# Performance work log

Hardware: AMD Instinct MI355X
Metric: run time of the kernel (lower is better)

Reference implementation:

```python
import jax, jax.numpy as jnp
import numpy as np

B = 8
C = 128          # channels
H = 1024         # sparse (hidden) channels in bottleneck
START = 128      # start_frames
SPARSE = 8192    # sparse_frames
K = 512          # k_sparse
N_UP = 6         # log2(SPARSE/START) upsample blocks
EPS = 1e-5


def conv1d(x, w, b, stride=1, pad=0):
    # x: (B, Cin, L), w: (Cout, Cin, K)
    y = jax.lax.conv_general_dilated(
        x, w, window_strides=(stride,), padding=[(pad, pad)],
        dimension_numbers=('NCW', 'OIW', 'NCW'))
    return y + b[None, :, None]


def batch_norm(x, g, beta):
    # training-mode BatchNorm1d: stats over (batch, length) per channel
    m = x.mean(axis=(0, 2), keepdims=True)
    v = x.var(axis=(0, 2), keepdims=True)
    return (x - m) * jax.lax.rsqrt(v + EPS) * g[None, :, None] + beta[None, :, None]


def lrelu(x):
    return jnp.where(x >= 0, x, 0.2 * x)


def setup_inputs() -> dict:
    key = jax.random.key(0)
    ks = jax.random.split(key, 16)
    s = 0.05
    return {
        'x': jax.random.normal(ks[0], (B, C, START), dtype=jnp.float32),
        'up_w': jax.random.normal(ks[1], (N_UP, C, C, 3), dtype=jnp.float32) * s,
        'up_b': jnp.zeros((N_UP, C), dtype=jnp.float32),
        'up_g': jnp.ones((N_UP, C), dtype=jnp.float32),
        'up_beta': jnp.zeros((N_UP, C), dtype=jnp.float32),
        'up_out_w': jax.random.normal(ks[2], (C, C, 3), dtype=jnp.float32) * s,
        'up_out_b': jnp.zeros((C,), dtype=jnp.float32),
        # SparseBottleneck 1x1 convs (stored as (out,in) matrices)
        'sb_up_w': jax.random.normal(ks[3], (H, C), dtype=jnp.float32) * s,
        'sb_up_b': jnp.zeros((H,), dtype=jnp.float32),
        'sal_w': jax.random.normal(ks[4], (H, C), dtype=jnp.float32) * s,
        'sal_b': jnp.zeros((H,), dtype=jnp.float32),
        'sb_down_w': jax.random.normal(ks[5], (C, H), dtype=jnp.float32) * s,
        'sb_down_b': jnp.zeros((C,), dtype=jnp.float32),
        'dn_w': jax.random.normal(ks[6], (3, C, C, 7), dtype=jnp.float32) * s,
        'dn_b': jnp.zeros((3, C), dtype=jnp.float32),
        'dn_g': jnp.ones((3, C), dtype=jnp.float32),
        'dn_beta': jnp.zeros((3, C), dtype=jnp.float32),
    }


def reference(x, up_w, up_b, up_g, up_beta, up_out_w, up_out_b,
              sb_up_w, sb_up_b, sal_w, sal_b, sb_down_w, sb_down_b,
              dn_w, dn_b, dn_g, dn_beta):
    # ---- ConvUpsample: 128 -> 8192 frames ----
    for i in range(N_UP):
        x = jnp.repeat(x, 2, axis=-1)
        x = conv1d(x, up_w[i], up_b[i], stride=1, pad=1)
        x = lrelu(batch_norm(x, up_g[i], up_beta[i]))
    x = conv1d(x, up_out_w, up_out_b, stride=1, pad=1)  # (B, C, 8192)

    # ---- SparseBottleneck ----
    sig = jnp.einsum('bcl,hc->bhl', x, sb_up_w) + sb_up_b[None, :, None]   # (B,H,L)
    sal = jnp.einsum('bcl,hc->bhl', x, sal_w) + sal_b[None, :, None]       # (B,H,L)
    flat = jax.nn.softmax(sal.reshape(B, -1), axis=-1)   # softmax over H*L
    vals, idx = jax.lax.top_k(flat, K)                   # (B, K)
    sparse = jnp.zeros_like(flat).at[jnp.arange(B)[:, None], idx].set(vals)
    sal = sparse.reshape(sal.shape)
    x = sig * sal                                         # gated, (B,H,L)
    x = jnp.einsum('bhl,ch->bcl', x, sb_down_w) + sb_down_b[None, :, None]

    # ---- down stack: 8192 -> 128 frames ----
    for i in range(3):
        x = conv1d(x, dn_w[i], dn_b[i], stride=4, pad=3)
        x = lrelu(x)
        x = batch_norm(x, dn_g[i], dn_beta[i])
    return x  # (B, C, 128)
```

## Files before the change

### kernel.cpp

```cpp
#include <hip/hip_runtime.h>
#include <hip/hip_bf16.h>


#define DEV_INLINE __device__ __forceinline__

constexpr int NB   = 8;
constexpr int NC   = 128;
constexpr int NH   = 1024;
constexpr int LFULL= 8192;
constexpr int KSEL = 512;
constexpr int CAP  = 32768;

typedef __attribute__((ext_vector_type(4))) float f32x4;
typedef __attribute__((ext_vector_type(8))) short bf16x8;

DEV_INLINE unsigned monoKey(float f) {
    unsigned u = __float_as_uint(f);
    return (u & 0x80000000u) ? ~u : (u | 0x80000000u);
}
DEV_INLINE float keyToF(unsigned k) {
    unsigned u = (k & 0x80000000u) ? (k ^ 0x80000000u) : ~k;
    return __uint_as_float(u);
}
DEV_INLINE unsigned monoKey16(unsigned u) {
    return (u & 0x8000u) ? ((~u) & 0xFFFFu) : (u | 0x8000u);
}
DEV_INLINE unsigned bf16r(float f) {
    unsigned u = __float_as_uint(f);
    return (u + 0x7FFFu + ((u >> 16) & 1u)) >> 16;
}
DEV_INLINE float lrelu(float v) { return v >= 0.f ? v : 0.2f * v; }
DEV_INLINE float f4c(const float4& v, int k) {
    return k == 0 ? v.x : k == 1 ? v.y : k == 2 ? v.z : v.w;
}
DEV_INLINE int swz4(int p) { return p ^ ((p >> 3) & 7); }

DEV_INLINE void loadg4(const float* __restrict__ rowp, int g0, int L, float* e) {
    if (g0 >= 0 && g0 + 4 <= L) {
        float4 v = *(const float4*)(rowp + g0);
        e[0] = v.x; e[1] = v.y; e[2] = v.z; e[3] = v.w;
    } else {
#pragma unroll
        for (int t = 0; t < 4; t++) {
            int g = g0 + t;
            e[t] = (g >= 0 && g < L) ? rowp[g] : 0.f;
        }
    }
}

__global__ __launch_bounds__(256) void prep_k(
    const float* __restrict__ up_w, const float* __restrict__ up_out_w,
    const float* __restrict__ dn_w, float* __restrict__ wprep)
{
    int idx = blockIdx.x * 256 + threadIdx.x;
    if (idx < 393216) {
        int layer = idx >> 16;
        int r0 = idx & 65535;
        int c = r0 >> 9, r = (r0 >> 7) & 3, o = r0 & 127;
        const float* wsrc = up_w + ((size_t)layer * 128 + o) * 384 + c * 3;
        float w0 = wsrc[0], w1 = wsrc[1], w2 = wsrc[2];
        wprep[idx] = (r == 0) ? w0 : (r == 1) ? (w1 + w2) : (r == 2) ? (w0 + w1) : w2;
    } else if (idx < 442368) {
        int r0 = idx - 393216;
        int c = r0 / 384, k = (r0 / 128) % 3, o = r0 & 127;
        wprep[idx] = up_out_w[((size_t)o * 128 + c) * 3 + k];
    } else {
        int r0 = idx - 442368;
        int layer = r0 / 114688;
        int r1 = r0 - layer * 114688;
        int c = r1 / 896, k = (r1 / 128) % 7, o = r1 & 127;
        wprep[idx] = dn_w[((size_t)layer * 128 + o) * 896 + c * 7 + k];
    }
}

__global__ __launch_bounds__(256) void prepA_k(
    const float* __restrict__ up_w, const float* __restrict__ up_out_w,
    unsigned short* __restrict__ afrag)
{
    int idx = blockIdx.x * 256 + threadIdx.x;
    if (idx >= 221184) return;
    int rid = idx >> 6, lane = idx & 63;
    const int r15 = lane & 15, g = lane >> 4;
    unsigned short vals[8];
    if (rid < 3072) {
        int L  = rid >> 9;
        int r0 = rid & 511;
        int f = r0 & 3, ks = (r0 >> 2) & 1, cc = (r0 >> 3) & 1;
        int wo = (r0 >> 4) & 1, half = (r0 >> 5) & 1, ptap = (r0 >> 6) & 3;
        int o = wo * 64 + f * 16 + r15;
        int cb = cc * 64 + ks * 32 + g * 8;
#pragma unroll
        for (int e = 0; e < 8; e++) {
            const float* ws = up_w + (((size_t)L * 128 + o) * 128 + (cb + e)) * 3;
            float w0 = ws[0], w1 = ws[1], w2 = ws[2];
            float v = (ptap == 0) ? w0 : (ptap == 1) ? (w1 + w2)
                    : (ptap == 2) ? (w0 + w1) : w2;
            unsigned hi = bf16r(v);
            if (half == 0) vals[e] = (unsigned short)hi;
            else vals[e] = (unsigned short)bf16r(v - __uint_as_float(hi << 16));
        }
    } else {
        int r2 = rid - 3072;
        int f = r2 & 3, ks = (r2 >> 2) & 1, cc = (r2 >> 3) & 1;
        int wo = (r2 >> 4) & 1, half = (r2 >> 5) & 1, tap = r2 >> 6;
        int o = wo * 64 + f * 16 + r15;
        int cb = cc * 64 + ks * 32 + g * 8;
#pragma unroll
        for (int e = 0; e < 8; e++) {
            float v = up_out_w[((size_t)o * 128 + (cb + e)) * 3 + tap];
            unsigned hi = bf16r(v);
            if (half == 0) vals[e] = (unsigned short)hi;
            else vals[e] = (unsigned short)bf16r(v - __uint_as_float(hi << 16));
        }
    }
    unsigned pk[4];
#pragma unroll
    for (int q = 0; q < 4; q++)
        pk[q] = (unsigned)vals[2*q] | ((unsigned)vals[2*q+1] << 16);
    *(uint4*)(afrag + (size_t)rid * 512 + lane * 8) = make_uint4(pk[0], pk[1], pk[2], pk[3]);
}

__global__ __launch_bounds__(256) void redstats_k(
    const float* __restrict__ partial, int nb, float* __restrict__ stats)
{
    const int c = threadIdx.x;
    float s0 = 0.f, s1 = 0.f, s2 = 0.f, s3 = 0.f;
    for (int i = blockIdx.x * 4; i < nb; i += gridDim.x * 4) {
        s0 += partial[(size_t)(i + 0) * 256 + c];
        s1 += partial[(size_t)(i + 1) * 256 + c];
        s2 += partial[(size_t)(i + 2) * 256 + c];
        s3 += partial[(size_t)(i + 3) * 256 + c];
    }
    float s = (s0 + s1) + (s2 + s3);
    if (s != 0.f || blockIdx.x == 0) atomicAdd(&stats[c], s);
}

template<int INMODE>
__global__ __launch_bounds__(512) void mconvU_k(
    const float* __restrict__ in, float* __restrict__ out,
    const unsigned short* __restrict__ afrag, const float* __restrict__ bias,
    const float* __restrict__ stp, const float* __restrict__ gp,
    const float* __restrict__ btp, float inv_n,
    float* __restrict__ partial, int L_in)
{
    __shared__ unsigned short Xh[66 * 64], Xl[66 * 64];
    __shared__ float scs[NC], shs[NC];
    __shared__ float sstat[256];

    const int b = blockIdx.y, tile0 = blockIdx.x * 64, tid = threadIdx.x;
    const int lane = tid & 63, wid = tid >> 6;
    const int wo = wid >> 2, par = (wid >> 1) & 1, jh = wid & 1;
    const int r15 = lane & 15, g = lane >> 4;
    const int bid = b * gridDim.x + blockIdx.x;

    if (tid < 256) sstat[tid] = 0.f;
    if (INMODE > 0) {
        for (int c = tid; c < NC; c += 512) {
            float m  = stp[c] * inv_n;
            float va = stp[NC + c] * inv_n - m * m;
            float sc = gp[c] * rsqrtf(va + 1e-5f);
            scs[c] = sc;
            shs[c] = btp[c] - m * sc;
        }
    }

    f32x4 acc[4][2];
#pragma unroll
    for (int i = 0; i < 4; i++)
#pragma unroll
        for (int j = 0; j < 2; j++) acc[i][j] = (f32x4)(0.f);

    for (int cc = 0; cc < 2; cc++) {
        __syncthreads();
        {
            int r = tid & 63;
            int l = tile0 - 1 + r;
            for (int c0 = (tid >> 6); c0 < 64; c0 += 8) {
                int c = cc * 64 + c0;
                float v = 0.f;
                if (l >= 0 && l < L_in) {
                    v = in[((size_t)b * NC + c) * L_in + l];
                    if (INMODE > 0) v = lrelu(v * scs[c] + shs[c]);
                }
                unsigned hi = bf16r(v);
                unsigned lo = bf16r(v - __uint_as_float(hi << 16));
                unsigned bo = ((unsigned)(r * 128 + c0 * 2)) ^ (((unsigned)(r & 7)) << 4);
                *(unsigned short*)((char*)Xh + bo) = (unsigned short)hi;
                *(unsigned short*)((char*)Xl + bo) = (unsigned short)lo;
            }
            if (tid < 128) {
                int r2 = 64 + (tid >> 6);
                int l2 = tile0 - 1 + r2;
                int c0 = tid & 63;
                int c = cc * 64 + c0;
                float v = 0.f;
                if (l2 >= 0 && l2 < L_in) {
                    v = in[((size_t)b * NC + c) * L_in + l2];
                    if (INMODE > 0) v = lrelu(v * scs[c] + shs[c]);
                }
                unsigned hi = bf16r(v);
                unsigned lo = bf16r(v - __uint_as_float(hi << 16));
                unsigned bo = ((unsigned)(r2 * 128 + c0 * 2)) ^ (((unsigned)(r2 & 7)) << 4);
                *(unsigned short*)((char*)Xh + bo) = (unsigned short)hi;
                *(unsigned short*)((char*)Xl + bo) = (unsigned short)lo;
            }
        }
        __syncthreads();
#pragma unroll
        for (int pt = 0; pt < 2; pt++) {
            const int ptap = par * 2 + pt;
            const int roff = (ptap == 0) ? 0 : (ptap == 3) ? 2 : 1;
#pragma unroll
            for (int combo = 0; combo < 3; combo++) {
                const int ah = (combo == 2) ? 1 : 0;
                const unsigned short* Xs = (combo == 1) ? Xl : Xh;
                bf16x8 af[8];
#pragma unroll
                for (int ks = 0; ks < 2; ks++)
#pragma unroll
                    for (int f = 0; f < 4; f++) {
                        int rec = ((((ptap * 2 + ah) * 2 + wo) * 2 + cc) * 2 + ks) * 4 + f;
                        af[ks * 4 + f] = *(const bf16x8*)(afrag + (size_t)rec * 512 + lane * 8);
                    }
#pragma unroll
                for (int ks = 0; ks < 2; ks++) {
                    bf16x8 bf_[2];
#pragma unroll
                    for (int j = 0; j < 2; j++) {
                        int row = (jh * 2 + j) * 16 + r15 + roff;
                        unsigned bo = ((unsigned)(row * 128 + ks * 64 + g * 16))
                                    ^ (((unsigned)(row & 7)) << 4);
                        bf_[j] = *(const bf16x8*)((const char*)Xs + bo);
                    }
#pragma unroll
                    for (int i = 0; i < 4; i++)
#pragma unroll
                        for (int j = 0; j < 2; j++)
                            acc[i][j] = __builtin_amdgcn_mfma_f32_16x16x32_bf16(
                                af[ks * 4 + i], bf_[j], acc[i][j], 0, 0, 0);
                }
            }
        }
    }

    const int L_out = 2 * L_in;
#pragma unroll
    for (int i = 0; i < 4; i++) {
#pragma unroll
        for (int r = 0; r < 4; r++) {
            const int o = wo * 64 + i * 16 + g * 4 + r;
            const float bv = bias[o];
            float s1 = 0.f, s2 = 0.f;
#pragma unroll
            for (int j = 0; j < 2; j++) {
                float v = acc[i][j][r] + bv;
                int lout = 2 * (tile0 + (jh * 2 + j) * 16 + r15) + par;
                out[((size_t)b * NC + o) * L_out + lout] = v;
                s1 += v; s2 += v * v;
            }
#pragma unroll
            for (int m = 1; m < 16; m <<= 1) {
                s1 += __shfl_xor(s1, m);
                s2 += __shfl_xor(s2, m);
            }
            if (r15 == 0) {
                atomicAdd(&sstat[o], s1);
                atomicAdd(&sstat[NC + o], s2);
            }
        }
    }
    __syncthreads();
    if (tid < 256) partial[(size_t)bid * 256 + tid] = sstat[tid];
}

__global__ __launch_bounds__(512) void mconvF_k(
    const float* __restrict__ in, float* __restrict__ out,
    const unsigned short* __restrict__ afrag, const float* __restrict__ bias,
    const float* __restrict__ stp, const float* __restrict__ gp,
    const float* __restrict__ btp, float inv_n,
    unsigned short* __restrict__ xtout)
{
    __shared__ unsigned short Xh[130 * 64], Xl[130 * 64];
    __shared__ float scs[NC], shs[NC];

    const int b = blockIdx.y, l0 = blockIdx.x * 128, tid = threadIdx.x;
    const int lane = tid & 63, wid = tid >> 6;
    const int wo = wid >> 2, wl = (wid & 3) * 32;
    const int r15 = lane & 15, g = lane >> 4;

    for (int c = tid; c < NC; c += 512) {
        float m  = stp[c] * inv_n;
        float va = stp[NC + c] * inv_n - m * m;
        float sc = gp[c] * rsqrtf(va + 1e-5f);
        scs[c] = sc;
        shs[c] = btp[c] - m * sc;
    }

    f32x4 acc[4][2];
#pragma unroll
    for (int i = 0; i < 4; i++)
#pragma unroll
        for (int j = 0; j < 2; j++) acc[i][j] = (f32x4)(0.f);

    for (int cc = 0; cc < 2; cc++) {
        __syncthreads();
        {
            int r = tid & 127;
            int l = l0 - 1 + r;
            for (int c0 = (tid >> 7); c0 < 64; c0 += 4) {
                int c = cc * 64 + c0;
                float v = 0.f;
                if (l >= 0 && l < LFULL) {
                    v = in[((size_t)b * NC + c) * LFULL + l];
                    v = lrelu(v * scs[c] + shs[c]);
                }
                unsigned hi = bf16r(v);
                unsigned lo = bf16r(v - __uint_as_float(hi << 16));
                unsigned bo = ((unsigned)(r * 128 + c0 * 2)) ^ (((unsigned)(r & 7)) << 4);
                *(unsigned short*)((char*)Xh + bo) = (unsigned short)hi;
                *(unsigned short*)((char*)Xl + bo) = (unsigned short)lo;
            }
            if (tid < 128) {
                int r2 = 128 + (tid >> 6);
                int l2 = l0 - 1 + r2;
                int c0 = tid & 63;
                int c = cc * 64 + c0;
                float v = 0.f;
                if (l2 >= 0 && l2 < LFULL) {
                    v = in[((size_t)b * NC + c) * LFULL + l2];
                    v = lrelu(v * scs[c] + shs[c]);
                }
                unsigned hi = bf16r(v);
                unsigned lo = bf16r(v - __uint_as_float(hi << 16));
                unsigned bo = ((unsigned)(r2 * 128 + c0 * 2)) ^ (((unsigned)(r2 & 7)) << 4);
                *(unsigned short*)((char*)Xh + bo) = (unsigned short)hi;
                *(unsigned short*)((char*)Xl + bo) = (unsigned short)lo;
            }
        }
        __syncthreads();
#pragma unroll
        for (int tap = 0; tap < 3; tap++) {
#pragma unroll
            for (int combo = 0; combo < 3; combo++) {
                const int ah = (combo == 2) ? 1 : 0;
                const unsigned short* Xs = (combo == 1) ? Xl : Xh;
                bf16x8 af[8];
#pragma unroll
                for (int ks = 0; ks < 2; ks++)
#pragma unroll
                    for (int f = 0; f < 4; f++) {
                        int rec = 3072 + ((((tap * 2 + ah) * 2 + wo) * 2 + cc) * 2 + ks) * 4 + f;
                        af[ks * 4 + f] = *(const bf16x8*)(afrag + (size_t)rec * 512 + lane * 8);
                    }
#pragma unroll
                for (int ks = 0; ks < 2; ks++) {
                    bf16x8 bf_[2];
#pragma unroll
                    for (int j = 0; j < 2; j++) {
                        int row = wl + j * 16 + r15 + tap;
                        unsigned bo = ((unsigned)(row * 128 + ks * 64 + g * 16))
                                    ^ (((unsigned)(row & 7)) << 4);
                        bf_[j] = *(const bf16x8*)((const char*)Xs + bo);
                    }
#pragma unroll
                    for (int i = 0; i < 4; i++)
#pragma unroll
                        for (int j = 0; j < 2; j++)
                            acc[i][j] = __builtin_amdgcn_mfma_f32_16x16x32_bf16(
                                af[ks * 4 + i], bf_[j], acc[i][j], 0, 0, 0);
                }
            }
        }
    }

#pragma unroll
    for (int i = 0; i < 4; i++) {
#pragma unroll
        for (int r = 0; r < 4; r++) {
            const int o = wo * 64 + i * 16 + g * 4 + r;
            const float bv = bias[o];
#pragma unroll
            for (int j = 0; j < 2; j++) {
                float v = acc[i][j][r] + bv;
                int l = l0 + wl + j * 16 + r15;
                out[((size_t)b * NC + o) * LFULL + l] = v;
                xtout[((size_t)b * LFULL + l) * NC + o] = (unsigned short)bf16r(v);
            }
        }
    }
}

template<int KW, int STRIDE, int PAD, bool UPS, int INMODE, bool OUTACT, bool STATS, int TT, bool XPOSE, int OCW>
__global__ __launch_bounds__(256) void conv7_k(
    const float* __restrict__ in, float* __restrict__ out,
    const float* __restrict__ wp, const float* __restrict__ bias,
    const float* __restrict__ stp, const float* __restrict__ gp,
    const float* __restrict__ btp, float inv_n,
    float* __restrict__ stats, unsigned short* __restrict__ xtout,
    int L_in, int L_out)
{
    constexpr int CC    = (KW == 7) ? 8 : 16;
    constexpr int PT    = 64 * TT;
    constexpr int TTO   = UPS ? 2 * TT : TT;
    constexpr int NWR   = UPS ? 4 : KW;
    constexpr int OCB   = 4 * OCW;
    constexpr int SPAN  = UPS ? (PT + 2) : ((PT - 1) * STRIDE + KW);
    constexpr int NCH   = (SPAN + 3) / 4;
    constexpr int NCH8  = (NCH + 7) & ~7;
    constexpr int XROW  = 4 * NCH8 + 4;
    constexpr int NLD   = (CC * NCH + 255) / 256;
    constexpr int XSPAN = UPS ? (TT + 2) : ((TT - 1) * STRIDE + KW);
    constexpr int STEP  = UPS ? TT : TT * STRIDE;
    constexpr int NWQ   = CC * NWR * (OCB / 4);
    static_assert((STEP & 3) == 0, "conv7 swizzle path requires STEP%4==0");
    static_assert(OCW == 4 || OCW == 8, "OCW must be 4 or 8");

    __shared__ float xs[CC][XROW];
    __shared__ float wls[CC * NWR * OCB];
    __shared__ float scs[NC], shs[NC];

    const int b = blockIdx.z, ocb = blockIdx.y, tid = threadIdx.x;
    const int t0 = blockIdx.x * PT, lane = tid & 63;
    const int wid = tid >> 6;
    const int oc0 = ocb * OCB + wid * OCW;
    const int gb = UPS ? (t0 - 1) : (t0 * STRIDE - PAD);

    if (INMODE > 0) {
        for (int c = tid; c < NC; c += 256) {
            float m  = stp[c] * inv_n;
            float va = stp[NC + c] * inv_n - m * m;
            float sc = gp[c] * rsqrtf(va + 1e-5f);
            scs[c] = sc;
            shs[c] = btp[c] - m * sc;
        }
        __syncthreads();
    }

    float acc[OCW][TTO];
#pragma unroll
    for (int i = 0; i < OCW; i++)
#pragma unroll
        for (int j = 0; j < TTO; j++) acc[i][j] = 0.f;

    float pre[NLD][4];

#define C7_STAGEW(CCBASE) do {                                              \
    for (int _u = tid; _u < NWQ; _u += 256) {                               \
        int _row = _u / (OCB / 4), _g8 = _u % (OCB / 4);                    \
        int _cl = _row / NWR, _t = _row % NWR;                              \
        ((float4*)wls)[_u] = *(const float4*)(wp +                          \
            ((size_t)((CCBASE) + _cl) * NWR + _t) * 128 + ocb * OCB + _g8 * 4); \
    }                                                                       \
} while (0)

#define C7_COMPCI(CI) do {                                                  \
    float _q[XSPAN];                                                        \
    const int _qb4 = lane * (STEP / 4);                                     \
    _Pragma("unroll")                                                       \
    for (int _u = 0; _u < XSPAN / 4; _u++) {                                \
        float4 _v = *(const float4*)&xs[CI][4 * swz4(_qb4 + _u)];           \
        _q[4*_u] = _v.x; _q[4*_u+1] = _v.y;                                 \
        _q[4*_u+2] = _v.z; _q[4*_u+3] = _v.w;                               \
    }                                                                       \
    if constexpr ((XSPAN & 3) != 0) {                                       \
        const int _pt = swz4(_qb4 + XSPAN / 4);                             \
        if constexpr ((XSPAN & 3) >= 2) {                                   \
            float2 _v = *(const float2*)&xs[CI][4 * _pt];                   \
            _q[(XSPAN & ~3)] = _v.x; _q[(XSPAN & ~3) + 1] = _v.y;           \
        }                                                                   \
        if constexpr ((XSPAN & 3) == 1)                                     \
            _q[XSPAN - 1] = xs[CI][4 * _pt];                                \
        else if constexpr ((XSPAN & 3) == 3)                                \
            _q[XSPAN - 1] = xs[CI][4 * _pt + 2];                            \
    }                                                                       \
    {                                                                       \
        _Pragma("unroll")                                                   \
        for (int _k = 0; _k < KW; _k++) {                                   \
            if constexpr (OCW == 8) {                                       \
                const float4 _w0 = *(const float4*)&wls[((CI) * NWR + _k) * OCB + wid * 8];     \
                const float4 _w1 = *(const float4*)&wls[((CI) * NWR + _k) * OCB + wid * 8 + 4]; \
                _Pragma("unroll")                                           \
                for (int _i = 0; _i < 8; _i++) {                            \
                    float _wv = f4c(_i < 4 ? _w0 : _w1, _i & 3);            \
                    _Pragma("unroll")                                       \
                    for (int _j = 0; _j < TT; _j++)                         \
                        acc[_i][_j] = fmaf(_wv, _q[_j * STRIDE + _k], acc[_i][_j]); \
                }                                                           \
            } else {                                                        \
                const float4 _w0 = *(const float4*)&wls[((CI) * NWR + _k) * OCB + wid * 4];     \
                _Pragma("unroll")                                           \
                for (int _i = 0; _i < 4; _i++) {                            \
                    float _wv = f4c(_w0, _i);                               \
                    _Pragma("unroll")                                       \
                    for (int _j = 0; _j < TT; _j++)                         \
                        acc[_i][_j] = fmaf(_wv, _q[_j * STRIDE + _k], acc[_i][_j]); \
                }                                                           \
            }                                                               \
        }                                                                   \
    }                                                                       \
} while (0)

#pragma unroll
    for (int u = 0; u < NLD; u++) {
        int idx = tid + u * 256;
        if (idx < CC * NCH) {
            int cl = idx / NCH, q = idx - cl * NCH;
            loadg4(in + ((size_t)b * NC + cl) * L_in, gb + 4 * q, L_in, pre[u]);
        }
    }
#pragma unroll
    for (int u = 0; u < NLD; u++) {
        int idx = tid + u * 256;
        if (idx < CC * NCH) {
            int cl = idx / NCH, q = idx - cl * NCH;
            int g0 = gb + 4 * q;
            float e[4];
#pragma unroll
            for (int t = 0; t < 4; t++) {
                float v = pre[u][t];
                if (INMODE > 0) {
                    int gg = g0 + t;
                    if (gg >= 0 && gg < L_in) {
                        float s = v * scs[cl] + shs[cl];
                        v = (INMODE == 2) ? lrelu(s) : s;
                    }
                }
                e[t] = v;
            }
            *(float4*)&xs[cl][4 * swz4(q)] = make_float4(e[0], e[1], e[2], e[3]);
        }
    }
    C7_STAGEW(0);
    __syncthreads();

    for (int cc = 0; cc < NC; cc += CC) {
        if (cc + CC < NC) {
#pragma unroll
            for (int u = 0; u < NLD; u++) {
                int idx = tid + u * 256;
                if (idx < CC * NCH) {
                    int cl = idx / NCH, q = idx - cl * NCH;
                    loadg4(in + ((size_t)b * NC + cc + CC + cl) * L_in,
                           gb + 4 * q, L_in, pre[u]);
                }
            }
        }
#pragma unroll
        for (int ci = 0; ci < CC; ci++) {
            C7_COMPCI(ci);
        }
        __syncthreads();
        if (cc + CC < NC) {
#pragma unroll
            for (int u = 0; u < NLD; u++) {
                int idx = tid + u * 256;
                if (idx < CC * NCH) {
                    int cl = idx / NCH, q = idx - cl * NCH;
                    int g0 = gb + 4 * q;
                    int c = cc + CC + cl;
                    float e[4];
#pragma unroll
                    for (int t = 0; t < 4; t++) {
                        float v = pre[u][t];
                        if (INMODE > 0) {
                            int gg = g0 + t;
                            if (gg >= 0 && gg < L_in) {
                                float s = v * scs[c] + shs[c];
                                v = (INMODE == 2) ? lrelu(s) : s;
                            }
                        }
                        e[t] = v;
                    }
                    *(float4*)&xs[cl][4 * swz4(q)] = make_float4(e[0], e[1], e[2], e[3]);
                }
            }
            C7_STAGEW(cc + CC);
            __syncthreads();
        }
    }
#undef C7_STAGEW
#undef C7_COMPCI

    const int po = t0 + lane * TTO;
#pragma unroll
    for (int i = 0; i < OCW; i++) {
        const int o = oc0 + i;
        const float bv = bias[o];
        float s1 = 0.f, s2 = 0.f;
        float tmpm[TTO];
#pragma unroll
        for (int j = 0; j < TTO; j++) {
            float v = acc[i][j] + bv;
            if (OUTACT) v = lrelu(v);
            tmpm[j] = v;
            if (STATS) { s1 += v; s2 += v * v; }
        }
        float* orow = out + ((size_t)b * NC + o) * L_out + po;
        if constexpr (TTO == 4)
            *(float4*)orow = make_float4(tmpm[0], tmpm[1], tmpm[2], tmpm[3]);
        else if constexpr (TTO == 2)
            *(float2*)orow = make_float2(tmpm[0], tmpm[1]);
        else
            orow[0] = tmpm[0];
        if (STATS) {
#pragma unroll
            for (int m = 1; m < 64; m <<= 1) {
                s1 += __shfl_xor(s1, m);
                s2 += __shfl_xor(s2, m);
            }
            if (lane == 0) {
                atomicAdd(&stats[o], s1);
                atomicAdd(&stats[NC + o], s2);
            }
        }
    }
}

__global__ __launch_bounds__(256) void cvtW_k(const float* __restrict__ W,
                                              unsigned short* __restrict__ Wbf)
{
    int i = blockIdx.x * 256 + threadIdx.x;
    const float4 a = *(const float4*)&W[i * 8];
    const float4 b = *(const float4*)&W[i * 8 + 4];
    unsigned pk[4];
    pk[0] = bf16r(a.x) | (bf16r(a.y) << 16);
    pk[1] = bf16r(a.z) | (bf16r(a.w) << 16);
    pk[2] = bf16r(b.x) | (bf16r(b.y) << 16);
    pk[3] = bf16r(b.z) | (bf16r(b.w) << 16);
    *(uint4*)&Wbf[i * 8] = make_uint4(pk[0], pk[1], pk[2], pk[3]);
}

template<int PHASE>
__global__ __launch_bounds__(256) void salM2_k(
    const unsigned short* __restrict__ xT, const unsigned short* __restrict__ Wbf,
    const float* __restrict__ bias, float* __restrict__ gsum,
    unsigned* __restrict__ ghist, const unsigned* __restrict__ thrv,
    unsigned* __restrict__ candcnt, unsigned* __restrict__ candI)
{
    __shared__ unsigned short Als[128 * 128];
    __shared__ unsigned short Bls[128 * 128];

    const int b  = blockIdx.z;
    const int h0 = blockIdx.y * 128;
    const int l0 = blockIdx.x * 128;
    const int tid = threadIdx.x;
    const int lane = tid & 63;
    const int wid = tid >> 6;
    const int wh = (wid >> 1) * 64;
    const int wl = (wid & 1) * 64;

    {
        const uint4* gA = (const uint4*)(Wbf + (size_t)h0 * NC);
        const uint4* gB = (const uint4*)(xT + ((size_t)b * LFULL + l0) * NC);
        char* cA = (char*)Als; char* cB = (char*)Bls;
        for (int i = tid; i < 2048; i += 256) {
            int row = i >> 4, q = i & 15;
            unsigned sw = (unsigned)(row * 256 + q * 16) ^ (((unsigned)(row & 7)) << 4);
            *(uint4*)(cA + sw) = gA[i];
        }
        for (int i = tid; i < 2048; i += 256) {
            int row = i >> 4, q = i & 15;
            unsigned sw = (unsigned)(row * 256 + q * 16) ^ (((unsigned)(row & 7)) << 4);
            *(uint4*)(cB + sw) = gB[i];
        }
    }
    __syncthreads();

    f32x4 acc[4][4];
#pragma unroll
    for (int i = 0; i < 4; i++)
#pragma unroll
        for (int j = 0; j < 4; j++) acc[i][j] = (f32x4)(0.f);

    const int r15 = lane & 15, g = lane >> 4;
#pragma unroll
    for (int ks = 0; ks < 4; ks++) {
        bf16x8 af[4], bfv[4];
#pragma unroll
        for (int f = 0; f < 4; f++) {
            int rowA = wh + f * 16 + r15;
            unsigned offA = (unsigned)(rowA * 256 + ks * 64 + g * 16)
                          ^ (((unsigned)(rowA & 7)) << 4);
            af[f] = *(const bf16x8*)((const char*)Als + offA);
            int rowB = wl + f * 16 + r15;
            unsigned offB = (unsigned)(rowB * 256 + ks * 64 + g * 16)
                          ^ (((unsigned)(rowB & 7)) << 4);
            bfv[f] = *(const bf16x8*)((const char*)Bls + offB);
        }
#pragma unroll
        for (int i = 0; i < 4; i++)
#pragma unroll
            for (int j = 0; j < 4; j++)
                acc[i][j] = __builtin_amdgcn_mfma_f32_16x16x32_bf16(
                    af[i], bfv[j], acc[i][j], 0, 0, 0);
    }

    if constexpr (PHASE == 0) {
        __syncthreads();
        unsigned* lhist = (unsigned*)Als;
        for (int i = tid; i < 8192; i += 256) lhist[i] = 0;
        __syncthreads();
        unsigned* myh = lhist + (tid & 1) * 4096;
        float expsum = 0.f;
#pragma unroll
        for (int i = 0; i < 4; i++) {
#pragma unroll
            for (int r = 0; r < 4; r++) {
                const int h = h0 + wh + i * 16 + g * 4 + r;
                const float bv = bias[h];
#pragma unroll
                for (int j = 0; j < 4; j++) {
                    float v = acc[i][j][r] + bv;
                    expsum += expf(v);
                    atomicAdd(&myh[monoKey16(bf16r(v)) >> 4], 1u);
                }
            }
        }
#pragma unroll
        for (int m = 1; m < 64; m <<= 1) expsum += __shfl_xor(expsum, m);
        float* red = (float*)Bls;
        if (lane == 0) red[wid] = expsum;
        __syncthreads();
        for (int i = tid; i < 4096; i += 256) {
            unsigned s = lhist[i] + lhist[4096 + i];
            if (s) atomicAdd(&ghist[b * 4096 + i], s);
        }
        if (tid == 0) atomicAdd(&gsum[b], red[0] + red[1] + red[2] + red[3]);
    } else {
        const unsigned thr = thrv[b * 2];
#pragma unroll
        for (int i = 0; i < 4; i++) {
#pragma unroll
            for (int r = 0; r < 4; r++) {
                const int h = h0 + wh + i * 16 + g * 4 + r;
                const float bv = bias[h];
#pragma unroll
                for (int j = 0; j < 4; j++) {
                    float v = acc[i][j][r] + bv;
                    bool pr = monoKey16(bf16r(v)) >= thr;
                    unsigned long long m = __ballot(pr);
                    if (m) {
                        int leader = __ffsll((unsigned long long)m) - 1;
                        int cnt = __popcll(m);
                        unsigned basepos = 0;
                        if (lane == leader)
                            basepos = atomicAdd(&candcnt[b], (unsigned)cnt);
                        basepos = __shfl(basepos, leader);
                        if (pr) {
                            int rr = __popcll(m & ((1ull << lane) - 1ull));
                            unsigned pos = basepos + (unsigned)rr;
                            if (pos < CAP) {
                                int l = l0 + wl + j * 16 + r15;
                                candI[b * CAP + pos] = (unsigned)((h << 13) | l);
                            }
                        }
                    }
                }
            }
        }
    }
}

__global__ __launch_bounds__(256) void scan2_k(
    const unsigned* __restrict__ ghist, unsigned* __restrict__ thrv)
{
    const int b = blockIdx.x, tid = threadIdx.x;
    __shared__ unsigned part[256];
    unsigned s = 0;
#pragma unroll
    for (int i = 0; i < 16; i++) s += ghist[b * 4096 + tid * 16 + i];
    part[tid] = s;
    __syncthreads();
    if (tid == 0) {
        unsigned cum = 0; int ch;
        for (ch = 255; ch >= 0; ch--) {
            if (cum + part[ch] >= KSEL) break;
            cum += part[ch];
        }
        int bin = 0;
        if (ch >= 0) {
            for (bin = ch * 16 + 15; bin > ch * 16; bin--) {
                unsigned c = ghist[b * 4096 + bin];
                if (cum + c >= KSEL) break;
                cum += c;
            }
        }
        int bcol = bin > 0 ? bin - 1 : 0;
        thrv[b * 2] = (unsigned)bcol << 4;
    }
}

__global__ __launch_bounds__(128) void recompute_k(
    const unsigned* __restrict__ candcnt, const unsigned* __restrict__ candI,
    const float* __restrict__ xu, const float* __restrict__ W,
    const float* __restrict__ bias, unsigned* __restrict__ candK)
{
    const int b = blockIdx.y;
    const unsigned cnt = min(candcnt[b], (unsigned)CAP);
    const int t = threadIdx.x;
    __shared__ float wsum[2];
    for (unsigned k = blockIdx.x; k < cnt; k += 1024) {
        unsigned e = candI[b * CAP + k];
        int h = e >> 13, l = e & 8191;
        float prod = W[h * NC + t] * xu[(b * NC + t) * LFULL + l];
#pragma unroll
        for (int m = 1; m < 64; m <<= 1) prod += __shfl_xor(prod, m);
        if ((t & 63) == 0) wsum[t >> 6] = prod;
        __syncthreads();
        if (t == 0) candK[b * CAP + k] = monoKey(wsum[0] + wsum[1] + bias[h]);
        __syncthreads();
    }
}

__global__ __launch_bounds__(256) void select2_k(
    const unsigned* __restrict__ candcnt, const unsigned* __restrict__ candK,
    const unsigned* __restrict__ candI,
    uint2* __restrict__ selected, unsigned* __restrict__ selcnt)
{
    const int b = blockIdx.x, tid = threadIdx.x;
    __shared__ unsigned h1[4096];
    __shared__ unsigned l2k[2048], l2i[2048];
    __shared__ unsigned part[256];
    __shared__ unsigned sh[8];

    const unsigned Nc = min(candcnt[b], (unsigned)CAP);
    const unsigned* kk = candK + b * CAP;
    const unsigned* ii = candI + b * CAP;
    uint2* sel = selected + b * KSEL;

    for (int i = tid; i < 4096; i += 256) h1[i] = 0;
    if (tid < 8) sh[tid] = 0;
    __syncthreads();
    for (unsigned i = tid; i < Nc; i += 256) atomicAdd(&h1[kk[i] >> 20], 1u);
    __syncthreads();
    {
        unsigned s = 0;
#pragma unroll
        for (int i = 0; i < 16; i++) s += h1[tid * 16 + i];
        part[tid] = s;
        __syncthreads();
        if (tid == 0) {
            unsigned cum = 0; int ch;
            for (ch = 255; ch >= 0; ch--) { if (cum + part[ch] >= KSEL) break; cum += part[ch]; }
            int bin = 0;
            if (ch >= 0)
                for (bin = ch * 16 + 15; bin > ch * 16; bin--) {
                    unsigned c = h1[bin];
                    if (cum + c >= KSEL) break;
                    cum += c;
                }
            sh[2] = (unsigned)bin; sh[3] = KSEL - cum;
        }
    }
    __syncthreads();
    const unsigned b1 = sh[2], need1 = sh[3];
    for (int i = tid; i < 1024; i += 256) h1[i] = 0;
    __syncthreads();
    for (unsigned i = tid; i < Nc; i += 256) {
        unsigned k = kk[i], bin = k >> 20;
        if (bin > b1) {
            unsigned p = atomicAdd(&sh[0], 1u);
            if (p < KSEL) sel[p] = make_uint2(k, ii[i]);
        } else if (bin == b1) {
            atomicAdd(&h1[(k >> 10) & 1023], 1u);
        }
    }
    __syncthreads();
    {
        unsigned s = 0;
#pragma unroll
        for (int i = 0; i < 4; i++) s += h1[tid * 4 + i];
        part[tid] = s;
        __syncthreads();
        if (tid == 0) {
            unsigned cum = 0; int ch;
            for (ch = 255; ch >= 0; ch--) { if (cum + part[ch] >= need1) break; cum += part[ch]; }
            int bin = 0;
            if (ch >= 0)
                for (bin = ch * 4 + 3; bin > ch * 4; bin--) {
                    unsigned c = h1[bin];
                    if (cum + c >= need1) break;
                    cum += c;
                }
            sh[4] = (unsigned)bin; sh[5] = need1 - cum;
        }
    }
    __syncthreads();
    const unsigned b2 = sh[4], need2 = sh[5];
    for (int i = tid; i < 1024; i += 256) h1[i] = 0;
    __syncthreads();
    for (unsigned i = tid; i < Nc; i += 256) {
        unsigned k = kk[i];
        if ((k >> 20) != b1) continue;
        unsigned mb = (k >> 10) & 1023;
        if (mb > b2) {
            unsigned p = atomicAdd(&sh[0], 1u);
            if (p < KSEL) sel[p] = make_uint2(k, ii[i]);
        } else if (mb == b2) {
            unsigned j = atomicAdd(&sh[1], 1u);
            if (j < 2048) { l2k[j] = k; l2i[j] = ii[i]; atomicAdd(&h1[k & 1023], 1u); }
        }
    }
    __syncthreads();
    const unsigned m2 = min(sh[1], 2048u);
    {
        unsigned s = 0;
#pragma unroll
        for (int i = 0; i < 4; i++) s += h1[tid * 4 + i];
        part[tid] = s;
        __syncthreads();
        if (tid == 0) {
            unsigned cum = 0; int ch;
            for (ch = 255; ch >= 0; ch--) { if (cum + part[ch] >= need2) break; cum += part[ch]; }
            int bin = 0;
            if (ch >= 0)
                for (bin = ch * 4 + 3; bin > ch * 4; bin--) {
                    unsigned c = h1[bin];
                    if (cum + c >= need2) break;
                    cum += c;
                }
            sh[6] = (unsigned)bin; sh[7] = need2 - cum;
        }
    }
    __syncthreads();
    const unsigned b3 = sh[6], need3 = sh[7];
    if (tid == 0) sh[1] = 0;
    __syncthreads();
    for (unsigned i = tid; i < m2; i += 256) {
        unsigned k = l2k[i], lb = k & 1023;
        if (lb > b3) {
            unsigned p = atomicAdd(&sh[0], 1u);
            if (p < KSEL) sel[p] = make_uint2(k, l2i[i]);
        } else if (lb == b3) {
            unsigned t = atomicAdd(&sh[1], 1u);
            if (t < need3) {
                unsigned p = atomicAdd(&sh[0], 1u);
                if (p < KSEL) sel[p] = make_uint2(k, l2i[i]);
            }
        }
    }
    __syncthreads();
    if (tid == 0) selcnt[b] = min(sh[0], (unsigned)KSEL);
}

__global__ __launch_bounds__(128) void scatter2_k(
    const uint2* __restrict__ selected, const unsigned* __restrict__ selcnt,
    const float* __restrict__ gsum, const float* __restrict__ xu,
    const float* __restrict__ upw, const float* __restrict__ upb,
    float* __restrict__ gval)
{
    const int b = blockIdx.y, kidx = blockIdx.x;
    if (kidx >= (int)selcnt[b]) return;
    const uint2 s = selected[b * KSEL + kidx];
    const float salv = keyToF(s.x);
    const unsigned idx = s.y;
    const int h = idx >> 13, l = idx & 8191;
    const int t = threadIdx.x;

    float prod = upw[h * NC + t] * xu[(b * NC + t) * LFULL + l];
#pragma unroll
    for (int m = 1; m < 64; m <<= 1) prod += __shfl_xor(prod, m);
    __shared__ float wsum[2];
    if ((t & 63) == 0) wsum[t >> 6] = prod;
    __syncthreads();
    if (t == 0) {
        const float sig = wsum[0] + wsum[1] + upb[h];
        gval[b * KSEL + kidx] = sig * (expf(salv) / gsum[b]);
    }
}

__global__ __launch_bounds__(128) void dnconst_k(
    const float* __restrict__ dn_w, const float* __restrict__ dnb,
    const float* __restrict__ dn_b0, float* __restrict__ cst)
{
    const int o = threadIdx.x;
    float accA = 0.f, accE = 0.f;
    for (int c = 0; c < NC; c++) {
        const float bv = dnb[c];
        const float* wp = dn_w + ((size_t)o * NC + c) * 7;
#pragma unroll
        for (int k = 0; k < 7; k++) {
            float w = wp[k];
            accA += w * bv;
            if (k >= 3) accE += w * bv;
        }
    }
    cst[o]       = accA + dn_b0[o];
    cst[NC + o]  = accE + dn_b0[o];
}

__global__ __launch_bounds__(256) void fillpre_k(
    const float* __restrict__ cst, float* __restrict__ pre)
{
    const int row = blockIdx.x;
    const int o = row & 127;
    const float vI = cst[o], v0 = cst[NC + o];
    float4* p = (float4*)(pre + (size_t)row * 2048);
#pragma unroll
    for (int u = 0; u < 2; u++) {
        int q = threadIdx.x + u * 256;
        float4 v = make_float4(vI, vI, vI, vI);
        if (q == 0) v.x = v0;
        p[q] = v;
    }
}

__global__ __launch_bounds__(128) void corrdn_k(
    const uint2* __restrict__ selected, const unsigned* __restrict__ selcnt,
    const float* __restrict__ gval, const float* __restrict__ dww,
    const float* __restrict__ w0p, float* __restrict__ pre)
{
    const int b = blockIdx.y, kidx = blockIdx.x;
    if (kidx >= (int)selcnt[b]) return;
    const unsigned idx = selected[b * KSEL + kidx].y;
    const int h = idx >> 13, l = idx & 8191;
    const float g = gval[b * KSEL + kidx];
    const int o = threadIdx.x;

    __shared__ float dlt[NC];
    dlt[o] = dww[o * NH + h] * g;
    __syncthreads();

    const int tlo = (l <= 3) ? 0 : ((l - 3 + 3) >> 2);
    const int thi = min(2047, (l + 3) >> 2);
    for (int t = tlo; t <= thi; t++) {
        const int k = l - 4 * t + 3;
        float corr = 0.f;
#pragma unroll 4
        for (int c = 0; c < NC; c++)
            corr += w0p[(size_t)c * 896 + k * 128 + o] * dlt[c];
        atomicAdd(&pre[((size_t)b * NC + o) * 2048 + t], corr);
    }
}

__global__ __launch_bounds__(256) void actstats_k(
    float* __restrict__ pre, float* __restrict__ stats)
{
    const int row = blockIdx.x;
    const int o = row & 127;
    float4* p = (float4*)(pre + (size_t)row * 2048);
    float s1 = 0.f, s2 = 0.f;
#pragma unroll
    for (int u = 0; u < 2; u++) {
        int q = threadIdx.x + u * 256;
        float4 v = p[q];
        float e[4] = {v.x, v.y, v.z, v.w};
#pragma unroll
        for (int t = 0; t < 4; t++) {
            float a = lrelu(e[t]);
            e[t] = a;
            s1 += a; s2 += a * a;
        }
        p[q] = make_float4(e[0], e[1], e[2], e[3]);
    }
#pragma unroll
    for (int m = 1; m < 64; m <<= 1) {
        s1 += __shfl_xor(s1, m);
        s2 += __shfl_xor(s2, m);
    }
    __shared__ float red[8];
    const int lane = threadIdx.x & 63, wid = threadIdx.x >> 6;
    if (lane == 0) { red[wid] = s1; red[4 + wid] = s2; }
    __syncthreads();
    if (threadIdx.x == 0) {
        atomicAdd(&stats[o],      red[0] + red[1] + red[2] + red[3]);
        atomicAdd(&stats[NC + o], red[4] + red[5] + red[6] + red[7]);
    }
}

__global__ void apply_k(const float* __restrict__ in, const float* __restrict__ stats,
                        const float* __restrict__ g, const float* __restrict__ bt,
                        float* __restrict__ out, float inv_n)
{
    int i = blockIdx.x * 256 + threadIdx.x;
    int c = (i >> 7) & 127;
    float m  = stats[c] * inv_n;
    float va = stats[NC + c] * inv_n - m * m;
    float sc = g[c] * rsqrtf(va + 1e-5f);
    out[i] = in[i] * sc + (bt[c] - m * sc);
}

extern "C" void kernel_launch(void* const* d_in, const int* in_sizes, int n_in,
                              void* d_out, int out_size, void* d_ws, size_t ws_size,
                              hipStream_t stream)
{
    const float* x        = (const float*)d_in[0];
    const float* up_w     = (const float*)d_in[1];
    const float* up_b     = (const float*)d_in[2];
    const float* up_g     = (const float*)d_in[3];
    const float* up_beta  = (const float*)d_in[4];
    const float* up_out_w = (const float*)d_in[5];
    const float* up_out_b = (const float*)d_in[6];
    const float* sb_up_w  = (const float*)d_in[7];
    const float* sb_up_b  = (const float*)d_in[8];
    const float* sal_w    = (const float*)d_in[9];
    const float* sal_b    = (const float*)d_in[10];
    const float* sb_dn_w  = (const float*)d_in[11];
    const float* sb_dn_b  = (const float*)d_in[12];
    const float* dn_w     = (const float*)d_in[13];
    const float* dn_b     = (const float*)d_in[14];
    const float* dn_g     = (const float*)d_in[15];
    const float* dn_beta  = (const float*)d_in[16];

    char* ws = (char*)d_ws;
    float*          stats    = (float*)(ws + 0);
    float*          gsum     = (float*)(ws + 16384);
    unsigned*       thrv     = (unsigned*)(ws + 16416);
    unsigned*       candcnt  = (unsigned*)(ws + 16480);
    unsigned*       selcnt   = (unsigned*)(ws + 16512);
    uint2*          selected = (uint2*)(ws + 16640);
    unsigned*       ghist    = (unsigned*)(ws + 49408);
    unsigned*       candK    = (unsigned*)(ws + 180480);
    unsigned*       candI    = (unsigned*)(ws + 1229056);
    unsigned short* Wbf      = (unsigned short*)(ws + 2277632);
    float*          wprep    = (float*)(ws + 2539776);
    float*          B0       = (float*)(ws + 5685504);
    float*          B1       = (float*)(ws + 39239936);
    unsigned short* xT       = (unsigned short*)(ws + 72794368);
    unsigned short* Afrag    = (unsigned short*)(ws + 117440512);
    float*          partial  = (float*)(ws + 121634816);
    float*          gval     = (float*)(ws + 122159104);
    float*          cst      = (float*)(ws + 122175488);

    hipMemsetAsync(d_ws, 0, 16544, stream);
    hipMemsetAsync(ws + 49408, 0, 131072, stream);

    cvtW_k<<<64,256,0,stream>>>(sal_w, Wbf);
    prep_k<<<3072,256,0,stream>>>(up_w, up_out_w, dn_w, wprep);
    prepA_k<<<864,256,0,stream>>>(up_w, up_out_w, Afrag);

    mconvU_k<0><<<dim3(2,NB),512,0,stream>>>(
        x, B0, Afrag, up_b, nullptr, nullptr, nullptr, 0.f, partial, 128);
    redstats_k<<<16,256,0,stream>>>(partial, 2*NB, stats);
    mconvU_k<2><<<dim3(4,NB),512,0,stream>>>(
        B0, B1, Afrag + 1*262144, up_b + NC,
        stats, up_g, up_beta, 1.f/(float)(NB*256), partial, 256);
    redstats_k<<<16,256,0,stream>>>(partial, 4*NB, stats + 256);
    mconvU_k<2><<<dim3(8,NB),512,0,stream>>>(
        B1, B0, Afrag + 2*262144, up_b + 2*NC,
        stats + 256, up_g + NC, up_beta + NC, 1.f/(float)(NB*512), partial, 512);
    redstats_k<<<16,256,0,stream>>>(partial, 8*NB, stats + 2*256);
    mconvU_k<2><<<dim3(16,NB),512,0,stream>>>(
        B0, B1, Afrag + 3*262144, up_b + 3*NC,
        stats + 2*256, up_g + 2*NC, up_beta + 2*NC, 1.f/(float)(NB*1024), partial, 1024);
    redstats_k<<<16,256,0,stream>>>(partial, 16*NB, stats + 3*256);
    mconvU_k<2><<<dim3(32,NB),512,0,stream>>>(
        B1, B0, Afrag + 4*262144, up_b + 4*NC,
        stats + 3*256, up_g + 3*NC, up_beta + 3*NC, 1.f/(float)(NB*2048), partial, 2048);
    redstats_k<<<16,256,0,stream>>>(partial, 32*NB, stats + 4*256);
    mconvU_k<2><<<dim3(64,NB),512,0,stream>>>(
        B0, B1, Afrag + 5*262144, up_b + 5*NC,
        stats + 4*256, up_g + 4*NC, up_beta + 4*NC, 1.f/(float)(NB*4096), partial, 4096);
    redstats_k<<<16,256,0,stream>>>(partial, 64*NB, stats + 5*256);
    mconvF_k<<<dim3(64,NB),512,0,stream>>>(
        B1, B0, Afrag, up_out_b,
        stats + 5*256, up_g + 5*NC, up_beta + 5*NC, 1.f/(float)(NB*LFULL), xT);

    salM2_k<0><<<dim3(64,8,NB),256,0,stream>>>(xT, Wbf, sal_b, gsum, ghist,
                                               nullptr, nullptr, nullptr);
    scan2_k<<<NB,256,0,stream>>>(ghist, thrv);
    salM2_k<1><<<dim3(64,8,NB),256,0,stream>>>(xT, Wbf, sal_b, nullptr, nullptr,
                                               thrv, candcnt, candI);
    recompute_k<<<dim3(1024,NB),128,0,stream>>>(candcnt, candI, B0, sal_w, sal_b, candK);
    select2_k<<<NB,256,0,stream>>>(candcnt, candK, candI, selected, selcnt);
    scatter2_k<<<dim3(KSEL,NB),128,0,stream>>>(selected, selcnt, gsum, B0,
                                               sb_up_w, sb_up_b, gval);

    dnconst_k<<<1,128,0,stream>>>(dn_w, sb_dn_b, dn_b, cst);
    fillpre_k<<<NB*NC,256,0,stream>>>(cst, B1);
    corrdn_k<<<dim3(KSEL,NB),128,0,stream>>>(selected, selcnt, gval, sb_dn_w,
                                             wprep + 442368, B1);
    actstats_k<<<NB*NC,256,0,stream>>>(B1, stats + 6*256);

    conv7_k<7,4,3,false,1,true,true,1,false,4><<<dim3(8,8,NB),256,0,stream>>>(
        B1, B0, wprep + 442368 + 114688, dn_b + NC,
        stats + 6*256, dn_g, dn_beta, 1.f/(float)(NB*2048),
        stats + 7*256, nullptr, 2048, 512);
    conv7_k<7,4,3,false,1,true,true,1,false,4><<<dim3(2,8,NB),256,0,stream>>>(
        B0, B1, wprep + 442368 + 2*114688, dn_b + 2*NC,
        stats + 7*256, dn_g + NC, dn_beta + NC, 1.f/(float)(NB*512),
        stats + 8*256, nullptr, 512, 128);

    apply_k<<<(out_size + 255)/256,256,0,stream>>>(
        B1, stats + 8*256, dn_g + 2*NC, dn_beta + 2*NC, (float*)d_out,
        1.f/(float)(NB*128));
}
```

Measured before the change: 655.5 us.

## Record per-tile max key in saliency pass and skip tiles below threshold

The first saliency GEMM pass now records the maximum 16-bit monotone key per 128x128 tile, and the second pass returns early for tiles whose maximum falls below the top-k threshold, skipping their GEMM. The LDS histogram is also split into four copies to cut atomic contention, and expf is replaced with the faster __expf intrinsic. The early exit is safe because a tile with every key below the threshold cannot produce candidates. The cost is a small extra workspace buffer and slightly less accurate exponentials.

After: 642.0 us. -2.0%, faster.

```diff
diff --git a/kernel.cpp b/kernel.cpp
--- a/kernel.cpp
+++ b/kernel.cpp
@@ -635,10 +635,13 @@
     const unsigned short* __restrict__ xT, const unsigned short* __restrict__ Wbf,
     const float* __restrict__ bias, float* __restrict__ gsum,
     unsigned* __restrict__ ghist, const unsigned* __restrict__ thrv,
-    unsigned* __restrict__ candcnt, unsigned* __restrict__ candI)
+    unsigned* __restrict__ candcnt, unsigned* __restrict__ candI,
+    unsigned* __restrict__ tilemax)
 {
     __shared__ unsigned short Als[128 * 128];
     __shared__ unsigned short Bls[128 * 128];
+    __shared__ float redsm[4];
+    __shared__ unsigned redmx[4];
 
     const int b  = blockIdx.z;
     const int h0 = blockIdx.y * 128;
@@ -648,6 +651,13 @@
     const int wid = tid >> 6;
     const int wh = (wid >> 1) * 64;
     const int wl = (wid & 1) * 64;
+    const int tileid = (b * 8 + blockIdx.y) * 64 + blockIdx.x;
+
+    unsigned thr = 0;
+    if (PHASE == 1) {
+        thr = thrv[b * 2];
+        if (tilemax[tileid] < thr) return;
+    }
 
     {
         const uint4* gA = (const uint4*)(Wbf + (size_t)h0 * NC);
@@ -697,11 +707,13 @@
 
     if constexpr (PHASE == 0) {
         __syncthreads();
-        unsigned* lhist = (unsigned*)Als;
-        for (int i = tid; i < 8192; i += 256) lhist[i] = 0;
-        __syncthreads();
-        unsigned* myh = lhist + (tid & 1) * 4096;
+        unsigned* hA = (unsigned*)Als;
+        unsigned* hB = (unsigned*)Bls;
+        for (int i = tid; i < 8192; i += 256) { hA[i] = 0; hB[i] = 0; }
+        __syncthreads();
+        unsigned* myh = ((tid & 2) ? hB : hA) + (tid & 1) * 4096;
         float expsum = 0.f;
+        unsigned maxk = 0;
 #pragma unroll
         for (int i = 0; i < 4; i++) {
 #pragma unroll
@@ -711,23 +723,30 @@
 #pragma unroll
                 for (int j = 0; j < 4; j++) {
                     float v = acc[i][j][r] + bv;
-                    expsum += expf(v);
-                    atomicAdd(&myh[monoKey16(bf16r(v)) >> 4], 1u);
-                }
-            }
-        }
-#pragma unroll
-        for (int m = 1; m < 64; m <<= 1) expsum += __shfl_xor(expsum, m);
-        float* red = (float*)Bls;
-        if (lane == 0) red[wid] = expsum;
+                    expsum += __expf(v);
+                    unsigned k16 = monoKey16(bf16r(v));
+                    maxk = max(maxk, k16);
+                    atomicAdd(&myh[k16 >> 4], 1u);
+                }
+            }
+        }
+#pragma unroll
+        for (int m = 1; m < 64; m <<= 1) {
+            expsum += __shfl_xor(expsum, m);
+            maxk = max(maxk, (unsigned)__shfl_xor((int)maxk, m));
+        }
+        if (lane == 0) { redsm[wid] = expsum; redmx[wid] = maxk; }
         __syncthreads();
         for (int i = tid; i < 4096; i += 256) {
-            unsigned s = lhist[i] + lhist[4096 + i];
+            unsigned s = hA[i] + hA[4096 + i] + hB[i] + hB[4096 + i];
             if (s) atomicAdd(&ghist[b * 4096 + i], s);
         }
-        if (tid == 0) atomicAdd(&gsum[b], red[0] + red[1] + red[2] + red[3]);
+        if (tid == 0) {
+            atomicAdd(&gsum[b], redsm[0] + redsm[1] + redsm[2] + redsm[3]);
+            unsigned mx = max(max(redmx[0], redmx[1]), max(redmx[2], redmx[3]));
+            tilemax[tileid] = mx;
+        }
     } else {
-        const unsigned thr = thrv[b * 2];
 #pragma unroll
         for (int i = 0; i < 4; i++) {
 #pragma unroll
@@ -965,7 +984,7 @@
     __syncthreads();
     if (t == 0) {
         const float sig = wsum[0] + wsum[1] + upb[h];
-        gval[b * KSEL + kidx] = sig * (expf(salv) / gsum[b]);
+        gval[b * KSEL + kidx] = sig * (__expf(salv) / gsum[b]);
     }
 }
 
@@ -1121,6 +1140,7 @@
     float*          partial  = (float*)(ws + 121634816);
     float*          gval     = (float*)(ws + 122159104);
     float*          cst      = (float*)(ws + 122175488);
+    unsigned*       tilemax  = (unsigned*)(ws + 122176512);
 
     hipMemsetAsync(d_ws, 0, 16544, stream);
     hipMemsetAsync(ws + 49408, 0, 131072, stream);
@@ -1157,10 +1177,10 @@
         stats + 5*256, up_g + 5*NC, up_beta + 5*NC, 1.f/(float)(NB*LFULL), xT);
 
     salM2_k<0><<<dim3(64,8,NB),256,0,stream>>>(xT, Wbf, sal_b, gsum, ghist,
-                                               nullptr, nullptr, nullptr);
+                                               nullptr, nullptr, nullptr, tilemax);
     scan2_k<<<NB,256,0,stream>>>(ghist, thrv);
     salM2_k<1><<<dim3(64,8,NB),256,0,stream>>>(xT, Wbf, sal_b, nullptr, nullptr,
-                                               thrv, candcnt, candI);
+                                               thrv, candcnt, candI, tilemax);
     recompute_k<<<dim3(1024,NB),128,0,stream>>>(candcnt, candI, B0, sal_w, sal_b, candK);
     select2_k<<<NB,256,0,stream>>>(candcnt, candK, candI, selected, selcnt);
     scatter2_k<<<dim3(KSEL,NB),128,0,stream>>>(selected, selcnt, gsum, B0,
```
